# Performance work log

Hardware: AMD Instinct MI355X
Metric: run time of the kernel (lower is better)

## Reference

```python
import jax, jax.numpy as jnp
import numpy as np

NUM_HEADS = 32
KV_HEADS = 8
HEAD_DIM = 128
ROPE_BASE = 10000.0

def apply_rope(x):
    # x: [B, H, S, D]
    B, H, S, D = x.shape
    inv_freq = 1.0 / (ROPE_BASE ** (jnp.arange(0, D, 2, dtype=jnp.float32) / D))  # [D/2]
    t = jnp.arange(S, dtype=jnp.float32)
    freqs = jnp.einsum('s,d->sd', t, inv_freq)                 # [S, D/2]
    emb = jnp.concatenate([freqs, freqs], axis=-1)             # [S, D]
    cos = jnp.cos(emb)[None, None, :, :].astype(x.dtype)
    sin = jnp.sin(emb)[None, None, :, :].astype(x.dtype)
    x1, x2 = x[..., : D // 2], x[..., D // 2 :]
    rotated = jnp.concatenate([-x2, x1], axis=-1)
    return x * cos + rotated * sin

def setup_inputs() -> dict:
    key = jax.random.key(0)
    ks = jax.random.split(key, 6)
    B, S, H = 1, 2048, 4096
    scale = 1.0 / np.sqrt(H)
    return {
        'hidden_states': jax.random.normal(ks[0], (B, S, H), jnp.float32),
        'attention_mask': jnp.zeros((B, S), jnp.float32),
        'Wq': jax.random.normal(ks[1], (H, NUM_HEADS * HEAD_DIM), jnp.float32) * scale,
        'Wk': jax.random.normal(ks[2], (H, KV_HEADS * HEAD_DIM), jnp.float32) * scale,
        'Wv': jax.random.normal(ks[3], (H, KV_HEADS * HEAD_DIM), jnp.float32) * scale,
        'Wo': jax.random.normal(ks[4], (NUM_HEADS * HEAD_DIM, H), jnp.float32) * scale,
    }

def reference(hidden_states, attention_mask, Wq, Wk, Wv, Wo):
    B, S, _ = hidden_states.shape
    groups = NUM_HEADS // KV_HEADS
    q = (hidden_states @ Wq).reshape(B, S, NUM_HEADS, HEAD_DIM).transpose(0, 2, 1, 3)  # [B,H,S,D]
    k = (hidden_states @ Wk).reshape(B, S, KV_HEADS, HEAD_DIM).transpose(0, 2, 1, 3)   # [B,KV,S,D]
    v = (hidden_states @ Wv).reshape(B, S, KV_HEADS, HEAD_DIM).transpose(0, 2, 1, 3)
    q = apply_rope(q)
    k = apply_rope(k)
    # GQA: repeat kv heads to match query heads
    k = jnp.repeat(k, groups, axis=1)  # [B,H,S,D]
    v = jnp.repeat(v, groups, axis=1)
    scale = 1.0 / jnp.sqrt(jnp.asarray(HEAD_DIM, q.dtype))
    scores = jnp.einsum('bhqd,bhkd->bhqk', q, k) * scale       # [B,H,S,S]
    scores = scores + attention_mask[:, None, None, :]
    attn = jax.nn.softmax(scores, axis=-1)
    out = jnp.einsum('bhqk,bhkd->bhqd', attn, v)               # [B,H,S,D]
    out = out.transpose(0, 2, 1, 3).reshape(B, S, NUM_HEADS * HEAD_DIM)
    return out @ Wo
```

## Files before the change

kernel.cpp:

```cpp
#include <hip/hip_runtime.h>
#include <hip/hip_bf16.h>

typedef __bf16 bf16_t;
typedef __bf16 bf16x8 __attribute__((ext_vector_type(8)));
typedef __bf16 bf16x4 __attribute__((ext_vector_type(4)));
typedef float f32x4 __attribute__((ext_vector_type(4)));
typedef float f32x16 __attribute__((ext_vector_type(16)));

#define LOG2E 1.4426950408889634f

__device__ __forceinline__ void gload_lds16(const void* g, void* l) {
  __builtin_amdgcn_global_load_lds((const __attribute__((address_space(1))) void*)g,
                                   (__attribute__((address_space(3))) void*)l, 16, 0, 0);
}

__device__ __forceinline__ unsigned pk_bf16(float a, float b) {
  unsigned r;
  asm("v_cvt_pk_bf16_f32 %0, %1, %2" : "=v"(r) : "v"(a), "v"(b));
  return r;
}

__device__ __forceinline__ void trcvt_body(const float* src, bf16_t* dst, int R,
                                           int C, int cx, int cy, int tx, int ty,
                                           float (*tile)[33], bool perm) {
  int c0 = cx * 32, r0 = cy * 32;
#pragma unroll
  for (int i = 0; i < 4; ++i)
    tile[ty + i * 8][tx] = src[(size_t)(r0 + ty + i * 8) * C + c0 + tx];
  __syncthreads();
#pragma unroll
  for (int i = 0; i < 4; ++i) {
    int rc = c0 + ty + i * 8;
    int r_out = rc;
    if (perm) {
      int dd = rc & 127;
      int q = (dd & 15) + (dd & 16) + (((dd >> 5) & 1) ? 64 : 0) + ((dd >> 6) ? 32 : 0);
      r_out = (rc & ~127) | q;
    }
    dst[(size_t)r_out * R + r0 + tx] = (bf16_t)tile[tx][ty + i * 8];
  }
}

__global__ __launch_bounds__(256) void prep_kernel(
    const float* __restrict__ hidden, const float* __restrict__ Wq,
    const float* __restrict__ Wk, const float* __restrict__ Wv,
    const float* __restrict__ Wo, bf16_t* __restrict__ hB,
    bf16_t* __restrict__ Wqt, bf16_t* __restrict__ Wkvt,
    bf16_t* __restrict__ Wot, float* __restrict__ cosT,
    float* __restrict__ sinT) {
  __shared__ float tile[32][33];
  const int bx = blockIdx.x;
  const int t = threadIdx.x;
  const int tx = t & 31, ty = t >> 5;
  if (bx < 4096) {
    int i = bx * 256 + t;
    const float4* s4 = (const float4*)hidden;
    float4 a = s4[2 * i], b = s4[2 * i + 1];
    bf16x8 o;
    o[0] = (bf16_t)a.x; o[1] = (bf16_t)a.y; o[2] = (bf16_t)a.z; o[3] = (bf16_t)a.w;
    o[4] = (bf16_t)b.x; o[5] = (bf16_t)b.y; o[6] = (bf16_t)b.z; o[7] = (bf16_t)b.w;
    *(bf16x8*)(hB + 8 * (size_t)i) = o;
  } else if (bx < 4608) {
    int i = (bx - 4096) * 256 + t;
    int s = i >> 6, d = i & 63;
    float ang = (float)s * powf(10000.0f, -(float)d * (1.0f / 64.0f));
    cosT[i] = cosf(ang);
    sinT[i] = sinf(ang);
  } else if (bx < 20992) {
    int j = bx - 4608;
    trcvt_body(Wq, Wqt, 4096, 4096, j % 128, j / 128, tx, ty, tile, true);
  } else if (bx < 25088) {
    int j = bx - 20992;
    trcvt_body(Wk, Wkvt, 4096, 1024, j % 32, j / 32, tx, ty, tile, true);
  } else if (bx < 29184) {
    int j = bx - 25088;
    trcvt_body(Wv, Wkvt + (size_t)1024 * 4096, 4096, 1024, j % 32, j / 32, tx, ty, tile, false);
  } else {
    int j = bx - 29184;
    trcvt_body(Wo, Wot, 4096, 4096, j % 128, j / 128, tx, ty, tile, false);
  }
}

__global__ __launch_bounds__(256) void trb_kernel(const bf16_t* __restrict__ src,
                                                  bf16_t* __restrict__ dst, int R, int C) {
  __shared__ bf16_t tile[32][33];
  int c0 = blockIdx.x * 32, r0 = blockIdx.y * 32;
  int tx = threadIdx.x, ty = threadIdx.y;
#pragma unroll
  for (int i = 0; i < 4; ++i)
    tile[ty + i * 8][tx] = src[(size_t)(r0 + ty + i * 8) * C + c0 + tx];
  __syncthreads();
#pragma unroll
  for (int i = 0; i < 4; ++i)
    dst[(size_t)(c0 + ty + i * 8) * R + r0 + tx] = tile[tx][ty + i * 8];
}

__global__ __launch_bounds__(512, 2) void proj_gemm_kernel(
    const bf16_t* __restrict__ A, const bf16_t* __restrict__ Wqt,
    const bf16_t* __restrict__ Wkvt, const float* __restrict__ cosT,
    const float* __restrict__ sinT, bf16_t* __restrict__ Qb,
    bf16_t* __restrict__ Kb, bf16_t* __restrict__ Vb) {
  constexpr int K = 4096;
  extern __shared__ unsigned char sMem[];
  const int bx = blockIdx.x;
  const int mt = bx & 7, nt = bx >> 3;
  const int bm = mt * 256;
  const bf16_t* Btb = (nt < 16) ? (Wqt + (size_t)nt * 256 * K)
                                : (Wkvt + (size_t)(nt - 16) * 256 * K);

  const int t = threadIdx.x;
  const int rowU = t >> 2;
  const int cole = ((t & 3) * 8) ^ ((rowU & 8) ? 16 : 0);
  const bf16_t* aS = A + (size_t)(bm + rowU) * K + cole;
  const bf16_t* bS = Btb + (size_t)rowU * K + cole;

  const int lane = t & 63, w = t >> 6;
  const int wm = w >> 2, wn = w & 3;
  const int lr = lane & 15, lq = lane >> 4;
  const int colb = (lq * 16) ^ ((lr & 8) ? 32 : 0);

  auto stA = [&](int c, int h, int j) {
    unsigned char* d = sMem + c * 65536 + h * 16384 + t * 16;
    const bf16_t* g = aS + (size_t)h * 128 * K + j * 64;
    gload_lds16(g, d);
    gload_lds16(g + 32, d + 8192);
  };
  auto stB = [&](int c, int h, int j) {
    unsigned char* d = sMem + c * 65536 + 32768 + h * 16384 + t * 16;
    const bf16_t* g = bS + (size_t)h * 128 * K + j * 64;
    gload_lds16(g, d);
    gload_lds16(g + 32, d + 8192);
  };
  auto LA = [&](int c, int half, int mi, int kk) {
    return *(const bf16x8*)(sMem + c * 65536 + wm * 16384 + kk * 8192 +
                            (half * 64 + mi * 16 + lr) * 64 + colb);
  };
  auto LB = [&](int c, int ni, int kk) {
    return *(const bf16x8*)(sMem + c * 65536 + 32768 + (wn >> 1) * 16384 + kk * 8192 +
                            ((wn & 1) * 64 + ni * 16 + lr) * 64 + colb);
  };

  f32x4 acc[8][4];
#pragma unroll
  for (int i = 0; i < 8; ++i)
#pragma unroll
    for (int n = 0; n < 4; ++n) acc[i][n] = f32x4{0.f, 0.f, 0.f, 0.f};

  stA(0, 0, 0); stA(0, 1, 0); stB(0, 0, 0); stB(0, 1, 0);
  stB(1, 0, 1); stB(1, 1, 1);
  asm volatile("s_waitcnt vmcnt(4)" ::: "memory");
  __builtin_amdgcn_s_barrier();
  __builtin_amdgcn_sched_barrier(0);

  bf16x8 af[4][2], bf[2][2], bf2[2][2];
  for (int j = 0; j < 64; ++j) {
    const int c = j & 1, cn = c ^ 1;
    const int jp1 = (j + 1 < 64) ? j + 1 : 63;
    const int jp2 = (j + 2 < 64) ? j + 2 : 63;
#pragma unroll
    for (int mi = 0; mi < 4; ++mi)
#pragma unroll
      for (int kk = 0; kk < 2; ++kk) af[mi][kk] = LA(c, 0, mi, kk);
#pragma unroll
    for (int ni = 0; ni < 2; ++ni)
#pragma unroll
      for (int kk = 0; kk < 2; ++kk) bf[ni][kk] = LB(c, ni, kk);
    stA(cn, 0, jp1);
    __builtin_amdgcn_s_barrier();
    __builtin_amdgcn_sched_barrier(0);
    __builtin_amdgcn_s_setprio(1);
#pragma unroll
    for (int kk = 0; kk < 2; ++kk)
#pragma unroll
      for (int mi = 0; mi < 4; ++mi)
#pragma unroll
        for (int ni = 0; ni < 2; ++ni)
          acc[mi][ni] = __builtin_amdgcn_mfma_f32_16x16x32_bf16(af[mi][kk], bf[ni][kk],
                                                                acc[mi][ni], 0, 0, 0);
    __builtin_amdgcn_s_setprio(0);
    __builtin_amdgcn_sched_barrier(0);
    __builtin_amdgcn_s_barrier();
#pragma unroll
    for (int ni = 0; ni < 2; ++ni)
#pragma unroll
      for (int kk = 0; kk < 2; ++kk) bf2[ni][kk] = LB(c, 2 + ni, kk);
    stA(cn, 1, jp1);
    __builtin_amdgcn_s_barrier();
    __builtin_amdgcn_sched_barrier(0);
    __builtin_amdgcn_s_setprio(1);
#pragma unroll
    for (int kk = 0; kk < 2; ++kk)
#pragma unroll
      for (int mi = 0; mi < 4; ++mi)
#pragma unroll
        for (int ni = 0; ni < 2; ++ni)
          acc[mi][2 + ni] = __builtin_amdgcn_mfma_f32_16x16x32_bf16(af[mi][kk], bf2[ni][kk],
                                                                    acc[mi][2 + ni], 0, 0, 0);
    __builtin_amdgcn_s_setprio(0);
    __builtin_amdgcn_sched_barrier(0);
    __builtin_amdgcn_s_barrier();
#pragma unroll
    for (int mi = 0; mi < 4; ++mi)
#pragma unroll
      for (int kk = 0; kk < 2; ++kk) af[mi][kk] = LA(c, 1, mi, kk);
    stB(c, 0, jp2);
    __builtin_amdgcn_s_barrier();
    __builtin_amdgcn_sched_barrier(0);
    __builtin_amdgcn_s_setprio(1);
#pragma unroll
    for (int kk = 0; kk < 2; ++kk)
#pragma unroll
      for (int mi = 0; mi < 4; ++mi)
#pragma unroll
        for (int ni = 0; ni < 2; ++ni)
          acc[4 + mi][2 + ni] = __builtin_amdgcn_mfma_f32_16x16x32_bf16(
              af[mi][kk], bf2[ni][kk], acc[4 + mi][2 + ni], 0, 0, 0);
    __builtin_amdgcn_s_setprio(0);
    __builtin_amdgcn_sched_barrier(0);
    __builtin_amdgcn_s_barrier();
    stB(c, 1, jp2);
    __builtin_amdgcn_sched_barrier(0);
    __builtin_amdgcn_s_setprio(1);
#pragma unroll
    for (int kk = 0; kk < 2; ++kk)
#pragma unroll
      for (int mi = 0; mi < 4; ++mi)
#pragma unroll
        for (int ni = 0; ni < 2; ++ni)
          acc[4 + mi][ni] = __builtin_amdgcn_mfma_f32_16x16x32_bf16(
              af[mi][kk], bf[ni][kk], acc[4 + mi][ni], 0, 0, 0);
    __builtin_amdgcn_s_setprio(0);
    asm volatile("s_waitcnt vmcnt(4)" ::: "memory");
    __builtin_amdgcn_sched_barrier(0);
    __builtin_amdgcn_s_barrier();
  }

  if (nt < 20) {
    const bool isQ = nt < 16;
    bf16_t* dst = isQ ? Qb : Kb;
    const int ld = isQ ? 4096 : 1024;
    const int hh = isQ ? (nt * 2 + (wn >> 1)) : ((nt - 16) * 2 + (wn >> 1));
    const float qs = isQ ? 0.12751743f : 1.0f;
    const int dbase = lr + 32 * (wn & 1);
#pragma unroll
    for (int half = 0; half < 2; ++half)
#pragma unroll
      for (int mi = 0; mi < 4; ++mi)
#pragma unroll
        for (int ni = 0; ni < 2; ++ni) {
          int d = dbase + 16 * ni;
#pragma unroll
          for (int r = 0; r < 4; ++r) {
            int srow = bm + wm * 128 + half * 64 + mi * 16 + lq * 4 + r;
            float cv = cosT[srow * 64 + d], sv = sinT[srow * 64 + d];
            float x1 = acc[half * 4 + mi][ni][r], x2 = acc[half * 4 + mi][ni + 2][r];
            dst[(size_t)srow * ld + hh * 128 + d] = (bf16_t)((x1 * cv - x2 * sv) * qs);
            dst[(size_t)srow * ld + hh * 128 + d + 64] = (bf16_t)((x2 * cv + x1 * sv) * qs);
          }
        }
  } else {
    const int col0 = (nt - 20) * 256 + wn * 64;
#pragma unroll
    for (int half = 0; half < 2; ++half)
#pragma unroll
      for (int mi = 0; mi < 4; ++mi)
#pragma unroll
        for (int ni = 0; ni < 4; ++ni)
#pragma unroll
          for (int r = 0; r < 4; ++r) {
            int srow = bm + wm * 128 + half * 64 + mi * 16 + lq * 4 + r;
            Vb[(size_t)srow * 1024 + col0 + ni * 16 + lr] =
                (bf16_t)acc[half * 4 + mi][ni][r];
          }
  }
}

__global__ __launch_bounds__(512, 2) void out_gemm_kernel(
    const bf16_t* __restrict__ A, const bf16_t* __restrict__ B0,
    float* __restrict__ Cout) {
  constexpr int K = 4096;
  extern __shared__ unsigned char sMem[];
  const int bx = blockIdx.x;
  const int mt = bx & 7, nt = bx >> 3;
  const int bm = mt * 256;
  const bf16_t* Bt = B0 + (size_t)nt * 128 * K;

  const int t = threadIdx.x;
  const int rowU = t >> 2;
  const int cole = ((t & 3) * 8) ^ ((rowU & 8) ? 16 : 0);
  const bf16_t* aS = A + (size_t)(bm + rowU) * K + cole;
  const bf16_t* bS = Bt + (size_t)rowU * K + cole;

  const int lane = t & 63, w = t >> 6;
  const int wm = w >> 2, wn = w & 3;
  const int lr = lane & 15, lq = lane >> 4;
  const int colb = (lq * 16) ^ ((lr & 8) ? 32 : 0);

  auto stA = [&](int c, int h, int j) {
    unsigned char* d = sMem + c * 49152 + h * 16384 + t * 16;
    const bf16_t* g = aS + (size_t)h * 128 * K + j * 64;
    gload_lds16(g, d);
    gload_lds16(g + 32, d + 8192);
  };
  auto stB = [&](int c, int j) {
    unsigned char* d = sMem + c * 49152 + 32768 + t * 16;
    const bf16_t* g = bS + j * 64;
    gload_lds16(g, d);
    gload_lds16(g + 32, d + 8192);
  };
  auto LA = [&](int c, int half, int mi, int kk) {
    return *(const bf16x8*)(sMem + c * 49152 + wm * 16384 + kk * 8192 +
                            (half * 64 + mi * 16 + lr) * 64 + colb);
  };
  auto LB = [&](int c, int ni, int kk) {
    return *(const bf16x8*)(sMem + c * 49152 + 32768 + kk * 8192 +
                            (wn * 32 + ni * 16 + lr) * 64 + colb);
  };

  f32x4 acc[8][2];
#pragma unroll
  for (int i = 0; i < 8; ++i)
#pragma unroll
    for (int n = 0; n < 2; ++n) acc[i][n] = f32x4{0.f, 0.f, 0.f, 0.f};

  stA(0, 0, 0); stA(0, 1, 0); stB(0, 0);
  stB(1, 1);
  asm volatile("s_waitcnt vmcnt(2)" ::: "memory");
  __builtin_amdgcn_s_barrier();
  __builtin_amdgcn_sched_barrier(0);

  bf16x8 af[4][2], bf0[2], bf1[2];
  for (int j = 0; j < 64; ++j) {
    const int c = j & 1, cn = c ^ 1;
    const int jp1 = (j + 1 < 64) ? j + 1 : 63;
    const int jp2 = (j + 2 < 64) ? j + 2 : 63;
#pragma unroll
    for (int mi = 0; mi < 4; ++mi)
#pragma unroll
      for (int kk = 0; kk < 2; ++kk) af[mi][kk] = LA(c, 0, mi, kk);
#pragma unroll
    for (int kk = 0; kk < 2; ++kk) bf0[kk] = LB(c, 0, kk);
    stA(cn, 0, jp1);
    __builtin_amdgcn_s_barrier();
    __builtin_amdgcn_sched_barrier(0);
    __builtin_amdgcn_s_setprio(1);
#pragma unroll
    for (int kk = 0; kk < 2; ++kk)
#pragma unroll
      for (int mi = 0; mi < 4; ++mi)
        acc[mi][0] = __builtin_amdgcn_mfma_f32_16x16x32_bf16(af[mi][kk], bf0[kk],
                                                             acc[mi][0], 0, 0, 0);
    __builtin_amdgcn_s_setprio(0);
    __builtin_amdgcn_sched_barrier(0);
    __builtin_amdgcn_s_barrier();
#pragma unroll
    for (int kk = 0; kk < 2; ++kk) bf1[kk] = LB(c, 1, kk);
    stA(cn, 1, jp1);
    __builtin_amdgcn_s_barrier();
    __builtin_amdgcn_sched_barrier(0);
    __builtin_amdgcn_s_setprio(1);
#pragma unroll
    for (int kk = 0; kk < 2; ++kk)
#pragma unroll
      for (int mi = 0; mi < 4; ++mi)
        acc[mi][1] = __builtin_amdgcn_mfma_f32_16x16x32_bf16(af[mi][kk], bf1[kk],
                                                             acc[mi][1], 0, 0, 0);
    __builtin_amdgcn_s_setprio(0);
    __builtin_amdgcn_sched_barrier(0);
    __builtin_amdgcn_s_barrier();
#pragma unroll
    for (int mi = 0; mi < 4; ++mi)
#pragma unroll
      for (int kk = 0; kk < 2; ++kk) af[mi][kk] = LA(c, 1, mi, kk);
    stB(c, jp2);
    __builtin_amdgcn_s_barrier();
    __builtin_amdgcn_sched_barrier(0);
    __builtin_amdgcn_s_setprio(1);
#pragma unroll
    for (int kk = 0; kk < 2; ++kk)
#pragma unroll
      for (int mi = 0; mi < 4; ++mi)
        acc[4 + mi][1] = __builtin_amdgcn_mfma_f32_16x16x32_bf16(af[mi][kk], bf1[kk],
                                                                 acc[4 + mi][1], 0, 0, 0);
    __builtin_amdgcn_s_setprio(0);
    __builtin_amdgcn_sched_barrier(0);
    __builtin_amdgcn_s_barrier();
    __builtin_amdgcn_s_setprio(1);
#pragma unroll
    for (int kk = 0; kk < 2; ++kk)
#pragma unroll
      for (int mi = 0; mi < 4; ++mi)
        acc[4 + mi][0] = __builtin_amdgcn_mfma_f32_16x16x32_bf16(af[mi][kk], bf0[kk],
                                                                 acc[4 + mi][0], 0, 0, 0);
    __builtin_amdgcn_s_setprio(0);
    asm volatile("s_waitcnt vmcnt(2)" ::: "memory");
    __builtin_amdgcn_sched_barrier(0);
    __builtin_amdgcn_s_barrier();
  }

#pragma unroll
  for (int half = 0; half < 2; ++half)
#pragma unroll
    for (int mi = 0; mi < 4; ++mi)
#pragma unroll
      for (int ni = 0; ni < 2; ++ni)
#pragma unroll
        for (int r = 0; r < 4; ++r) {
          int row = bm + wm * 128 + half * 64 + mi * 16 + lq * 4 + r;
          Cout[(size_t)row * 4096 + nt * 128 + wn * 32 + ni * 16 + lr] =
              acc[half * 4 + mi][ni][r];
        }
}

__global__ __launch_bounds__(512) void attn_kernel(
    const bf16_t* __restrict__ Qb, const bf16_t* __restrict__ Kb,
    const bf16_t* __restrict__ Vt, const float* __restrict__ mask,
    bf16_t* __restrict__ Ob) {
  extern __shared__ unsigned char sMem[];
  const int bx = blockIdx.x;
  const int h = bx >> 3, qt = bx & 7;
  const int kvh = h >> 2;
  const int t = threadIdx.x, lane = t & 63, w = t >> 6;
  const int ln = lane & 31, hi = lane >> 5;
  const int q0 = qt * 256 + w * 32;
  const int swz = (ln & 7) << 4;

  bf16x8 qf[8];
#pragma unroll
  for (int ds = 0; ds < 8; ++ds)
    qf[ds] = *(const bf16x8*)(Qb + (size_t)(q0 + ln) * 4096 + h * 128 + ds * 16 + hi * 8);

  const int krow = t >> 4, kg = t & 15;
  const bf16_t* kSrc = Kb + (size_t)krow * 1024 + kvh * 128 +
                       (((kg * 16) ^ ((krow & 7) << 4)) >> 1);
  const int vrow = t >> 3, vg = t & 7;
  const bf16_t* vSrc = Vt + (size_t)(kvh * 128 + vrow) * 2048 +
                       (((vg * 16) ^ ((vrow & 7) << 4)) >> 1);

  auto stage = [&](int c, int kt) {
    unsigned char* kD = sMem + c * 16384 + t * 16;
    unsigned char* vD = sMem + 32768 + c * 16384 + t * 16;
    gload_lds16(kSrc + (size_t)kt * 64 * 1024, kD);
    gload_lds16(kSrc + (size_t)(kt * 64 + 32) * 1024, kD + 8192);
    gload_lds16(vSrc + kt * 64, vD);
    gload_lds16(vSrc + (size_t)64 * 2048 + kt * 64, vD + 8192);
  };

  f32x16 o[4];
#pragma unroll
  for (int db = 0; db < 4; ++db)
#pragma unroll
    for (int e = 0; e < 16; ++e) o[db][e] = 0.f;
  float mrun = -1e30f, lp = 0.f;

  stage(0, 0);
  gload_lds16(mask + t * 4, sMem + 65536 + t * 16);
  asm volatile("s_waitcnt vmcnt(0)" ::: "memory");
  __builtin_amdgcn_s_barrier();
  __builtin_amdgcn_sched_barrier(0);

  for (int kt = 0; kt < 32; ++kt) {
    const int c = kt & 1;
    if (kt < 31) {
      stage(c ^ 1, kt + 1);
      asm volatile("s_waitcnt vmcnt(4)" ::: "memory");
    } else {
      asm volatile("s_waitcnt vmcnt(0)" ::: "memory");
    }
    __builtin_amdgcn_s_barrier();
    __builtin_amdgcn_sched_barrier(0);

    const unsigned char* sK = sMem + c * 16384;
    const unsigned char* sV = sMem + 32768 + c * 16384;
    const unsigned char* sMk = sMem + 65536 + kt * 256;

#pragma unroll
    for (int sub = 0; sub < 2; ++sub) {
      f32x16 s;
#pragma unroll
      for (int e = 0; e < 16; ++e) s[e] = 0.f;
      __builtin_amdgcn_s_setprio(1);
#pragma unroll
      for (int ds = 0; ds < 8; ++ds) {
        bf16x8 kf = *(const bf16x8*)(sK + (sub * 32 + ln) * 256 +
                                     ((ds * 32 + hi * 16) ^ swz));
        s = __builtin_amdgcn_mfma_f32_32x32x16_bf16(kf, qf[ds], s, 0, 0, 0);
      }
      __builtin_amdgcn_s_setprio(0);
#pragma unroll
      for (int rg = 0; rg < 4; ++rg) {
        float4 mv = *(const float4*)(sMk + (sub * 32 + rg * 8 + 4 * hi) * 4);
        s[rg * 4 + 0] += LOG2E * mv.x; s[rg * 4 + 1] += LOG2E * mv.y;
        s[rg * 4 + 2] += LOG2E * mv.z; s[rg * 4 + 3] += LOG2E * mv.w;
      }
      float pm = s[0];
#pragma unroll
      for (int e = 1; e < 16; ++e) pm = fmaxf(pm, s[e]);
      pm = fmaxf(pm, __shfl_xor(pm, 32));
      if (!__all(pm - mrun <= 11.5f)) {
        float nm = fmaxf(mrun, pm);
        float al = exp2f(mrun - nm);
        mrun = nm;
        lp *= al;
#pragma unroll
        for (int db = 0; db < 4; ++db)
#pragma unroll
          for (int e = 0; e < 16; ++e) o[db][e] *= al;
      }
      float p[16], ps = 0.f;
#pragma unroll
      for (int e = 0; e < 16; ++e) {
        p[e] = exp2f(s[e] - mrun);
        ps += p[e];
      }
      lp += ps;
#pragma unroll
      for (int hh = 0; hh < 2; ++hh) {
        unsigned w0 = pk_bf16(p[8 * hh + 0], p[8 * hh + 1]);
        unsigned w1 = pk_bf16(p[8 * hh + 2], p[8 * hh + 3]);
        unsigned w2 = pk_bf16(p[8 * hh + 4], p[8 * hh + 5]);
        unsigned w3 = pk_bf16(p[8 * hh + 6], p[8 * hh + 7]);
        unsigned pw0 = __shfl_xor((int)w0, 32), pw1 = __shfl_xor((int)w1, 32);
        unsigned pw2 = __shfl_xor((int)w2, 32), pw3 = __shfl_xor((int)w3, 32);
        union { unsigned u[4]; bf16x8 v; } pf;
        pf.u[0] = hi ? pw2 : w0;
        pf.u[1] = hi ? pw3 : w1;
        pf.u[2] = hi ? w2 : pw0;
        pf.u[3] = hi ? w3 : pw1;
        __builtin_amdgcn_s_setprio(1);
#pragma unroll
        for (int db = 0; db < 4; ++db) {
          bf16x8 vf = *(const bf16x8*)(sV + (db * 32 + ln) * 128 +
                                       ((sub * 64 + hh * 32 + hi * 16) ^ swz));
          o[db] = __builtin_amdgcn_mfma_f32_32x32x16_bf16(vf, pf.v, o[db], 0, 0, 0);
        }
        __builtin_amdgcn_s_setprio(0);
      }
    }
    __builtin_amdgcn_s_barrier();
    __builtin_amdgcn_sched_barrier(0);
  }

  float l = lp + __shfl_xor(lp, 32);
  float inv = 1.0f / l;
  bf16_t* orow = Ob + (size_t)(q0 + ln) * 4096 + h * 128;
#pragma unroll
  for (int db = 0; db < 4; ++db)
#pragma unroll
    for (int rg = 0; rg < 4; ++rg) {
      bf16x4 ov;
#pragma unroll
      for (int j = 0; j < 4; ++j) ov[j] = (bf16_t)(o[db][rg * 4 + j] * inv);
      *(bf16x4*)(orow + db * 32 + rg * 8 + hi * 4) = ov;
    }
}

extern "C" void kernel_launch(void* const* d_in, const int* in_sizes, int n_in,
                              void* d_out, int out_size, void* d_ws, size_t ws_size,
                              hipStream_t stream) {
  const float* hidden = (const float*)d_in[0];
  const float* mask = (const float*)d_in[1];
  const float* Wq = (const float*)d_in[2];
  const float* Wk = (const float*)d_in[3];
  const float* Wv = (const float*)d_in[4];
  const float* Wo = (const float*)d_in[5];
  float* out = (float*)d_out;
  char* ws = (char*)d_ws;

  bf16_t* hB   = (bf16_t*)(ws + 0);
  bf16_t* Wqt  = (bf16_t*)(ws + 16777216);
  bf16_t* Wkvt = (bf16_t*)(ws + 50331648);
  bf16_t* Wot  = (bf16_t*)(ws + 67108864);
  bf16_t* Qb   = (bf16_t*)(ws + 100663296);
  bf16_t* Kb   = (bf16_t*)(ws + 117440512);
  bf16_t* Vb   = (bf16_t*)(ws + 121634816);
  bf16_t* Vt   = (bf16_t*)(ws + 125829120);
  bf16_t* Ob   = (bf16_t*)(ws + 130023424);
  float*  cosT = (float*)(ws + 146800640);
  float*  sinT = (float*)(ws + 147324928);

  hipFuncSetAttribute((const void*)attn_kernel,
                      hipFuncAttributeMaxDynamicSharedMemorySize, 73728);
  hipFuncSetAttribute((const void*)proj_gemm_kernel,
                      hipFuncAttributeMaxDynamicSharedMemorySize, 131072);
  hipFuncSetAttribute((const void*)out_gemm_kernel,
                      hipFuncAttributeMaxDynamicSharedMemorySize, 98304);

  prep_kernel<<<45568, 256, 0, stream>>>(hidden, Wq, Wk, Wv, Wo, hB, Wqt, Wkvt,
                                         Wot, cosT, sinT);
  proj_gemm_kernel<<<192, 512, 131072, stream>>>(hB, Wqt, Wkvt, cosT, sinT, Qb, Kb, Vb);
  trb_kernel<<<dim3(32, 64), dim3(32, 8), 0, stream>>>(Vb, Vt, 2048, 1024);
  attn_kernel<<<256, 512, 73728, stream>>>(Qb, Kb, Vt, mask, Ob);
  out_gemm_kernel<<<256, 512, 98304, stream>>>(Ob, Wot, out);
}
```

Before: 325.4 us.

## Overlap Wo transpose-convert with projection GEMM using extra idle-CU blocks

Moves the fp32-to-bf16 transpose of Wo out of the prep kernel and into 64 extra blocks appended to the projection GEMM launch. The GEMM uses only 192 blocks on a GPU with more CUs, so the spare CUs can do the Wo conversion at the same time. This shortens the prep kernel's serial bandwidth-bound work. The risk is that each new block handles a whole 64-column strip serially with 64 syncs, so it may run longer than the GEMM and become the tail, and it competes with the GEMM for memory bandwidth.

```diff
diff --git a/kernel.cpp b/kernel.cpp
--- a/kernel.cpp
+++ b/kernel.cpp
@@ -44,9 +44,8 @@
 __global__ __launch_bounds__(256) void prep_kernel(
     const float* __restrict__ hidden, const float* __restrict__ Wq,
     const float* __restrict__ Wk, const float* __restrict__ Wv,
-    const float* __restrict__ Wo, bf16_t* __restrict__ hB,
-    bf16_t* __restrict__ Wqt, bf16_t* __restrict__ Wkvt,
-    bf16_t* __restrict__ Wot, float* __restrict__ cosT,
+    bf16_t* __restrict__ hB, bf16_t* __restrict__ Wqt,
+    bf16_t* __restrict__ Wkvt, float* __restrict__ cosT,
     float* __restrict__ sinT) {
   __shared__ float tile[32][33];
   const int bx = blockIdx.x;
@@ -72,12 +71,9 @@
   } else if (bx < 25088) {
     int j = bx - 20992;
     trcvt_body(Wk, Wkvt, 4096, 1024, j % 32, j / 32, tx, ty, tile, true);
-  } else if (bx < 29184) {
+  } else {
     int j = bx - 25088;
     trcvt_body(Wv, Wkvt + (size_t)1024 * 4096, 4096, 1024, j % 32, j / 32, tx, ty, tile, false);
-  } else {
-    int j = bx - 29184;
-    trcvt_body(Wo, Wot, 4096, 4096, j % 128, j / 128, tx, ty, tile, false);
   }
 }
 
@@ -99,16 +95,35 @@
     const bf16_t* __restrict__ A, const bf16_t* __restrict__ Wqt,
     const bf16_t* __restrict__ Wkvt, const float* __restrict__ cosT,
     const float* __restrict__ sinT, bf16_t* __restrict__ Qb,
-    bf16_t* __restrict__ Kb, bf16_t* __restrict__ Vb) {
+    bf16_t* __restrict__ Kb, bf16_t* __restrict__ Vb,
+    const float* __restrict__ Wo, bf16_t* __restrict__ Wot) {
   constexpr int K = 4096;
   extern __shared__ unsigned char sMem[];
   const int bx = blockIdx.x;
+  const int t = threadIdx.x;
+
+  if (bx >= 192) {
+    float(*tl)[65] = (float(*)[65])sMem;
+    const int c0 = (bx - 192) * 64;
+    const int tc = t & 63, tr = t >> 6;
+    for (int r0 = 0; r0 < 4096; r0 += 64) {
+#pragma unroll
+      for (int i = 0; i < 8; ++i)
+        tl[tr + 8 * i][tc] = Wo[(size_t)(r0 + tr + 8 * i) * 4096 + c0 + tc];
+      __syncthreads();
+#pragma unroll
+      for (int i = 0; i < 8; ++i)
+        Wot[(size_t)(c0 + tr + 8 * i) * 4096 + r0 + tc] = (bf16_t)tl[tc][tr + 8 * i];
+      __syncthreads();
+    }
+    return;
+  }
+
   const int mt = bx & 7, nt = bx >> 3;
   const int bm = mt * 256;
   const bf16_t* Btb = (nt < 16) ? (Wqt + (size_t)nt * 256 * K)
                                 : (Wkvt + (size_t)(nt - 16) * 256 * K);
 
-  const int t = threadIdx.x;
   const int rowU = t >> 2;
   const int cole = ((t & 3) * 8) ^ ((rowU & 8) ? 16 : 0);
   const bf16_t* aS = A + (size_t)(bm + rowU) * K + cole;
@@ -586,9 +601,10 @@
   hipFuncSetAttribute((const void*)out_gemm_kernel,
                       hipFuncAttributeMaxDynamicSharedMemorySize, 98304);
 
-  prep_kernel<<<45568, 256, 0, stream>>>(hidden, Wq, Wk, Wv, Wo, hB, Wqt, Wkvt,
-                                         Wot, cosT, sinT);
-  proj_gemm_kernel<<<192, 512, 131072, stream>>>(hB, Wqt, Wkvt, cosT, sinT, Qb, Kb, Vb);
+  prep_kernel<<<29184, 256, 0, stream>>>(hidden, Wq, Wk, Wv, hB, Wqt, Wkvt,
+                                         cosT, sinT);
+  proj_gemm_kernel<<<256, 512, 131072, stream>>>(hB, Wqt, Wkvt, cosT, sinT,
+                                                 Qb, Kb, Vb, Wo, Wot);
   trb_kernel<<<dim3(32, 64), dim3(32, 8), 0, stream>>>(Vb, Vt, 2048, 1024);
   attn_kernel<<<256, 512, 73728, stream>>>(Qb, Kb, Vt, mask, Ob);
   out_gemm_kernel<<<256, 512, 98304, stream>>>(Ob, Wot, out);
```

Measured after the change: 313.2 us. 1.04x faster.
